# Performance work log

Hardware: AMD Instinct MI355X
Metric: run time of the kernel (lower is better)

Reference implementation:

```python
import jax, jax.numpy as jnp
import numpy as np

N_SRC, N_DST, N_EDGES = 50000, 50000, 500000
IN_DIM, OUT_DIM, EDGE_DIM = 128, 128, 11
BN_EPS = 1e-5


def setup_inputs() -> dict:
    key = jax.random.key(0)
    ks = jax.random.split(key, 16)
    s = 0.05
    return {
        "src_feat": jax.random.normal(ks[0], (N_SRC, IN_DIM), jnp.float32),
        "dst_feat": jax.random.normal(ks[1], (N_DST, IN_DIM), jnp.float32),
        "edge_feats": jax.random.normal(ks[2], (N_EDGES, EDGE_DIM), jnp.float32),
        "src_idx": jax.random.randint(ks[3], (N_EDGES,), 0, N_SRC, jnp.int32),
        "dst_idx": jax.random.randint(ks[4], (N_EDGES,), 0, N_DST, jnp.int32),
        "W_src": jax.random.normal(ks[5], (IN_DIM, OUT_DIM), jnp.float32) * s,
        "b_src": jnp.zeros((OUT_DIM,), jnp.float32),
        "W_dst": jax.random.normal(ks[6], (IN_DIM, OUT_DIM), jnp.float32) * s,
        "b_dst": jnp.zeros((OUT_DIM,), jnp.float32),
        "W_edge": jax.random.normal(ks[7], (EDGE_DIM, OUT_DIM), jnp.float32) * s,
        "b_edge": jnp.zeros((OUT_DIM,), jnp.float32),
        "attn_w": jax.random.normal(ks[8], (3 * OUT_DIM,), jnp.float32) * s,
        "attn_b": jnp.zeros((), jnp.float32),
        "gamma": jnp.ones((OUT_DIM,), jnp.float32),
        "beta": jnp.zeros((OUT_DIM,), jnp.float32),
        "alpha": jnp.asarray(0.25, jnp.float32),
    }


def reference(src_feat, dst_feat, edge_feats, src_idx, dst_idx,
              W_src, b_src, W_dst, b_dst, W_edge, b_edge,
              attn_w, attn_b, gamma, beta, alpha):
    D = W_src.shape[1]
    # project at node/edge level (math identical to projecting gathered feats)
    hs = src_feat @ W_src + b_src            # [Ns, D]  (linear_src)
    hd = dst_feat @ W_dst + b_dst            # [Nd, D]  (linear_dst)
    ep = edge_feats @ W_edge + b_edge        # [E, D]   (linear_edge)
    # attn_l on concat([src, dst, edge]) == sum of three dot products + bias
    aw_s, aw_d, aw_e = attn_w[:D], attn_w[D:2 * D], attn_w[2 * D:]
    a = (hs @ aw_s)[src_idx] + (hd @ aw_d)[dst_idx] + ep @ aw_e + attn_b  # [E]
    # edge softmax over incoming edges of each dst node
    n_dst = dst_feat.shape[0]
    seg_max = jax.ops.segment_max(a, dst_idx, num_segments=n_dst)
    a_exp = jnp.exp(a - seg_max[dst_idx])
    denom = jax.ops.segment_sum(a_exp, dst_idx, num_segments=n_dst)
    attn = a_exp / denom[dst_idx]            # [E]
    # weighted message = attn * linear_src(src_h); scatter-sum to dst
    msg = attn[:, None] * hs[src_idx]        # [E, D]
    h_new = jax.ops.segment_sum(msg, dst_idx, num_segments=n_dst)  # [Nd, D]
    # BatchNorm1d (training-mode batch statistics)
    mean = jnp.mean(h_new, axis=0)
    var = jnp.var(h_new, axis=0)
    h_bn = (h_new - mean) / jnp.sqrt(var + BN_EPS) * gamma + beta
    # PReLU (single shared alpha); dropout is identity in eval
    return jnp.where(h_bn >= 0, h_bn, alpha * h_bn)
```

## Files before the change

### kernel.cpp

```cpp
#include <hip/hip_runtime.h>
#include <cstddef>

#define NSRC 50000
#define NDST 50000
#define NEDGE 500000
#define DIM 128
#define EDIM 11
#define BN_EPS 1e-5f
#define SCAN_NBLK ((NDST + 255) / 256)

#define HS_BLOCKS ((NSRC + 63) / 64)
#define SCB       ((NSRC + 127) / 128)
#define EDB       ((NEDGE + 511) / 512)
#define SC_BLOCKS ((NEDGE + 1023) / 1024)
#define FUSE_GRID (196 * 13)

typedef short bf16x8 __attribute__((ext_vector_type(8)));
typedef float f32x4 __attribute__((ext_vector_type(4)));

#define OFF_HS       0
#define OFF_SSCORE   (OFF_HS + (size_t)NSRC*DIM/2)
#define OFF_DSCORE   (OFF_SSCORE + NSRC)
#define OFF_DEG16    (OFF_DSCORE + NDST)
#define OFF_COLSUM   (OFF_DEG16 + (size_t)NDST*16)
#define OFF_COLSQ    (OFF_COLSUM + 128)
#define OFF_OFFS     (OFF_COLSQ + 128)
#define OFF_EER      (OFF_OFFS + NDST + 2)
#define OFF_PAIRS    (OFF_EER + 2*(size_t)NEDGE)
#define OFF_WDVEC    (OFF_PAIRS + 2*(size_t)NEDGE)
#define OFF_WEVEC    (OFF_WDVEC + 128)
#define OFF_SCAL     (OFF_WEVEC + 16)
#define OFF_WSVEC    (OFF_SCAL + 4)
#define OFF_PART     (OFF_WSVEC + 128)
#define OFF_WT       (((OFF_PART + 256 + 3) / 4) * 4)

__device__ __forceinline__ unsigned short f2bf(float x) {
    unsigned int u = __float_as_uint(x);
    u += 0x7FFFu + ((u >> 16) & 1u);
    return (unsigned short)(u >> 16);
}
__device__ __forceinline__ float bf2f(unsigned int u16) {
    return __uint_as_float(u16 << 16);
}

__global__ __launch_bounds__(256) void k_prepwt(const float* __restrict__ W_dst,
                                                const float* __restrict__ b_dst,
                                                const float* __restrict__ W_edge,
                                                const float* __restrict__ b_edge,
                                                const float* __restrict__ W_src,
                                                const float* __restrict__ b_src,
                                                const float* __restrict__ attn_w,
                                                const float* __restrict__ attn_b,
                                                float* __restrict__ wd_vec,
                                                float* __restrict__ we_vec,
                                                float* __restrict__ ws_vec,
                                                float* __restrict__ scal,
                                                unsigned short* __restrict__ wt) {
    int bb = blockIdx.x;
    int t = threadIdx.x;
    __shared__ float red[128];
    __shared__ float tile[32][33];
    if (bb == 0) {
        if (t < 128) {
            float acc = 0.f;
            for (int d = 0; d < DIM; ++d) acc += W_dst[t * DIM + d] * attn_w[DIM + d];
            wd_vec[t] = acc;
            red[t] = b_dst[t] * attn_w[DIM + t];
        }
        __syncthreads();
        for (int s = 64; s > 0; s >>= 1) { if (t < s) red[t] += red[t + s]; __syncthreads(); }
        if (t == 0) scal[0] = red[0];
    } else if (bb == 1) {
        if (t < 128) {
            if (t < EDIM) {
                float e = 0.f;
                for (int d = 0; d < DIM; ++d) e += W_edge[t * DIM + d] * attn_w[2 * DIM + d];
                we_vec[t] = e;
            }
            red[t] = b_edge[t] * attn_w[2 * DIM + t];
        }
        __syncthreads();
        for (int s = 64; s > 0; s >>= 1) { if (t < s) red[t] += red[t + s]; __syncthreads(); }
        if (t == 0) scal[1] = red[0] + attn_b[0];
    } else if (bb == 2) {
        if (t < 128) {
            float acc = 0.f;
            for (int d = 0; d < DIM; ++d) acc += W_src[t * DIM + d] * attn_w[d];
            ws_vec[t] = acc;
            red[t] = b_src[t] * attn_w[t];
        }
        __syncthreads();
        for (int s = 64; s > 0; s >>= 1) { if (t < s) red[t] += red[t + s]; __syncthreads(); }
        if (t == 0) scal[2] = red[0];
    } else {
        int idx = bb - 3;
        int bi = idx & 3;
        int bj = idx >> 2;
        int cl = t & 31;
        #pragma unroll
        for (int i = 0; i < 4; ++i) {
            int kl = (t >> 5) * 4 + i;
            tile[kl][cl] = W_src[(size_t)(bi * 32 + kl) * DIM + bj * 32 + cl];
        }
        __syncthreads();
        int ko = t & 31;
        #pragma unroll
        for (int i = 0; i < 4; ++i) {
            int co = (t >> 5) * 4 + i;
            wt[(size_t)(bj * 32 + co) * DIM + bi * 32 + ko] = f2bf(tile[ko][co]);
        }
    }
}

__global__ __launch_bounds__(256, 2) void k_fused(const float* __restrict__ A,
                                               const unsigned short* __restrict__ wt,
                                               const float* __restrict__ bias,
                                               const float* __restrict__ ef,
                                               const float* __restrict__ dst_feat,
                                               const int* __restrict__ dst_idx,
                                               const float* __restrict__ ws_vec,
                                               const float* __restrict__ wd_vec,
                                               const float* __restrict__ we_vec,
                                               const float* __restrict__ scal,
                                               unsigned short* __restrict__ hsb,
                                               float* __restrict__ s_score,
                                               float* __restrict__ d_score,
                                               int2* __restrict__ eer,
                                               int* __restrict__ deg16) {
    const int g = blockIdx.x / 13;
    const int sl = blockIdx.x % 13;
    const int t = threadIdx.x;

    if (sl < 4) {
        const int hb = g * 4 + sl;
        if (hb >= HS_BLOCKS) return;
        const int wv = t >> 6;
        const int lane = t & 63;
        const int lrow = lane & 15;
        const int kg = lane >> 4;
        const int grow = hb * 64 + wv * 16 + lrow;
        const bool rowok = grow < NSRC;
        const float* arow = A + (size_t)grow * DIM;

        bf16x8 af[4];
        #pragma unroll
        for (int s = 0; s < 4; ++s) {
            float4 p0 = make_float4(0.f, 0.f, 0.f, 0.f), p1 = p0;
            if (rowok) {
                p0 = *reinterpret_cast<const float4*>(arow + 32 * s + kg * 8);
                p1 = *reinterpret_cast<const float4*>(arow + 32 * s + kg * 8 + 4);
            }
            bf16x8 a;
            a[0] = (short)f2bf(p0.x); a[1] = (short)f2bf(p0.y);
            a[2] = (short)f2bf(p0.z); a[3] = (short)f2bf(p0.w);
            a[4] = (short)f2bf(p1.x); a[5] = (short)f2bf(p1.y);
            a[6] = (short)f2bf(p1.z); a[7] = (short)f2bf(p1.w);
            af[s] = a;
        }

        f32x4 acc[8];
        #pragma unroll
        for (int c = 0; c < 8; ++c) acc[c] = (f32x4){0.f, 0.f, 0.f, 0.f};

        #pragma unroll
        for (int c = 0; c < 8; ++c) {
            #pragma unroll
            for (int s = 0; s < 4; ++s) {
                const bf16x8 b = *reinterpret_cast<const bf16x8*>(
                    wt + ((size_t)(16 * c + lrow) * DIM + 32 * s + kg * 8));
                acc[c] = __builtin_amdgcn_mfma_f32_16x16x32_bf16(af[s], b, acc[c], 0, 0, 0);
            }
        }

        const int orow0 = hb * 64 + wv * 16 + kg * 4;
        #pragma unroll
        for (int c = 0; c < 8; ++c) {
            float bb = bias[16 * c + lrow];
            #pragma unroll
            for (int i = 0; i < 4; ++i) {
                unsigned int mybf = f2bf(acc[c][i] + bb);
                unsigned int nb = (unsigned int)__shfl_xor((int)mybf, 1);
                int orow = orow0 + i;
                if ((lrow & 1) == 0 && orow < NSRC) {
                    *reinterpret_cast<unsigned int*>(hsb + (size_t)orow * DIM + 16 * c + lrow)
                        = (mybf & 0xFFFFu) | (nb << 16);
                }
            }
        }
    } else if (sl < 8) {
        int idx = g * 4 + (sl - 4);
        const float* X;
        const float* V;
        float* out;
        float c;
        if (idx < SCB) {
            X = A; V = ws_vec; out = s_score; c = scal[2];
        } else {
            idx -= SCB;
            if (idx >= SCB) return;
            X = dst_feat; V = wd_vec; out = d_score; c = scal[0];
        }
        int row = idx * 128 + (t >> 1);
        int c0 = (t & 1) * 64;
        if (row >= NDST) return;
        const float4* x = reinterpret_cast<const float4*>(X + (size_t)row * DIM + c0);
        const float4* w = reinterpret_cast<const float4*>(V + c0);
        float p = 0.f;
        #pragma unroll
        for (int i = 0; i < 16; ++i) {
            float4 a = x[i], b = w[i];
            p += a.x * b.x + a.y * b.y + a.z * b.z + a.w * b.w;
        }
        p += __shfl_xor(p, 1);
        if ((t & 1) == 0) out[row] = p + c;
    } else {
        const int eb = g * 5 + (sl - 8);
        if (eb >= EDB) return;
        float wvv[EDIM];
        #pragma unroll
        for (int k = 0; k < EDIM; ++k) wvv[k] = we_vec[k];
        const float s1 = scal[1];
        int ebase = eb * 512 + t;
        #pragma unroll
        for (int i = 0; i < 2; ++i) {
            int e = ebase + i * 256;
            if (e < NEDGE) {
                int d = dst_idx[e];
                const float* er = ef + (size_t)e * EDIM;
                float a = s1;
                #pragma unroll
                for (int k = 0; k < EDIM; ++k) a += er[k] * wvv[k];
                int r = atomicAdd(&deg16[(size_t)d * 16], 1);
                eer[e] = make_int2(r, __float_as_int(a));
            }
        }
    }
}

__global__ __launch_bounds__(256) void k_scanA(const int* __restrict__ deg16,
                                               int* __restrict__ offL,
                                               int* __restrict__ partials) {
    __shared__ int tmp[256];
    int t = threadIdx.x;
    int i = blockIdx.x * 256 + t;
    int v = (i < NDST) ? deg16[(size_t)i * 16] : 0;
    tmp[t] = v;
    __syncthreads();
    #pragma unroll
    for (int d = 1; d < 256; d <<= 1) {
        int u = (t >= d) ? tmp[t - d] : 0;
        __syncthreads();
        tmp[t] += u;
        __syncthreads();
    }
    if (i < NDST) offL[i] = tmp[t] - v;
    if (t == 255) partials[blockIdx.x] = tmp[255];
}

__global__ __launch_bounds__(256) void k_scanB(int* __restrict__ partials) {
    __shared__ int tmp[256];
    int t = threadIdx.x;
    int v = (t < SCAN_NBLK) ? partials[t] : 0;
    tmp[t] = v;
    __syncthreads();
    #pragma unroll
    for (int d = 1; d < 256; d <<= 1) {
        int u = (t >= d) ? tmp[t - d] : 0;
        __syncthreads();
        tmp[t] += u;
        __syncthreads();
    }
    if (t < SCAN_NBLK) partials[t] = tmp[t] - v;
}

__global__ __launch_bounds__(256) void k_scat(const int* __restrict__ src_idx,
                                              const int* __restrict__ dst_idx,
                                              const int2* __restrict__ eer,
                                              const float* __restrict__ s_score,
                                              const float* __restrict__ d_score,
                                              const int* __restrict__ offL,
                                              const int* __restrict__ part,
                                              int2* __restrict__ pairs) {
    int base = blockIdx.x * 1024 + threadIdx.x;
    #pragma unroll
    for (int i = 0; i < 4; ++i) {
        int e = base + i * 256;
        if (e < NEDGE) {
            int s = src_idx[e], d = dst_idx[e];
            int2 re = eer[e];
            float w = expf(__int_as_float(re.y) + s_score[s] + d_score[d]);
            int pos = offL[d] + part[d >> 8] + re.x;
            pairs[pos] = make_int2(s, __float_as_int(w));
        }
    }
}

__global__ __launch_bounds__(256) void k_gather(const unsigned short* __restrict__ hsb,
                                                const int* __restrict__ offL,
                                                const int* __restrict__ part,
                                                const int2* __restrict__ pairs,
                                                float* __restrict__ h_new) {
    int wid = (blockIdx.x * blockDim.x + threadIdx.x) >> 6;
    int lane = threadIdx.x & 63;
    if (wid >= NDST) return;
    int b = offL[wid] + part[wid >> 8];
    int e2 = (wid + 1 < NDST) ? (offL[wid + 1] + part[(wid + 1) >> 8]) : NEDGE;
    int deg = e2 - b;
    const int half = lane >> 5;
    const int c8 = lane & 31;
    float a0 = 0.f, a1 = 0.f, a2 = 0.f, a3 = 0.f, wsum = 0.f;

    for (int base = 0; base < deg; base += 64) {
        int cnt = min(deg - base, 64);
        int myS = 0;
        float myW = 0.f;
        if (lane < cnt) {
            int2 p = pairs[b + base + lane];
            myS = p.x;
            myW = __int_as_float(p.y);
        }
        wsum += myW;

        int j = 0;
        for (; j + 8 <= cnt; j += 8) {
            #pragma unroll
            for (int q = 0; q < 4; ++q) {
                int jj = j + 2 * q + half;
                int s0 = __shfl(myS, jj);
                float w0 = __shfl(myW, jj);
                uint2 v = *reinterpret_cast<const uint2*>(hsb + (size_t)s0 * DIM + c8 * 4);
                a0 += w0 * bf2f(v.x & 0xFFFFu);
                a1 += w0 * bf2f(v.x >> 16);
                a2 += w0 * bf2f(v.y & 0xFFFFu);
                a3 += w0 * bf2f(v.y >> 16);
            }
        }
        for (; j < cnt; j += 2) {
            int jj = j + half;
            int s0 = __shfl(myS, jj);
            float w0 = __shfl(myW, jj);
            uint2 v = *reinterpret_cast<const uint2*>(hsb + (size_t)s0 * DIM + c8 * 4);
            a0 += w0 * bf2f(v.x & 0xFFFFu);
            a1 += w0 * bf2f(v.x >> 16);
            a2 += w0 * bf2f(v.y & 0xFFFFu);
            a3 += w0 * bf2f(v.y >> 16);
        }
    }

    a0 += __shfl_xor(a0, 32);
    a1 += __shfl_xor(a1, 32);
    a2 += __shfl_xor(a2, 32);
    a3 += __shfl_xor(a3, 32);
    #pragma unroll
    for (int m = 1; m < 64; m <<= 1) wsum += __shfl_xor(wsum, m);

    float inv = (deg > 0) ? 1.f / wsum : 0.f;
    if (half == 0) {
        reinterpret_cast<float4*>(h_new + (size_t)wid * DIM)[c8]
            = make_float4(a0 * inv, a1 * inv, a2 * inv, a3 * inv);
    }
}

__global__ __launch_bounds__(256) void k_bnstats(const float* __restrict__ h,
                                                 float* __restrict__ colsum,
                                                 float* __restrict__ colsq) {
    int col = threadIdx.x & 127;
    int rp = threadIdx.x >> 7;
    float s = 0.f, q = 0.f;
    for (int r = blockIdx.x * 2 + rp; r < NDST; r += gridDim.x * 2) {
        float x = h[(size_t)r * DIM + col];
        s += x;
        q += x * x;
    }
    __shared__ float ls[2][128], lq[2][128];
    ls[rp][col] = s;
    lq[rp][col] = q;
    __syncthreads();
    if (rp == 0) {
        atomicAdd(&colsum[col], ls[0][col] + ls[1][col]);
        atomicAdd(&colsq[col], lq[0][col] + lq[1][col]);
    }
}

__global__ __launch_bounds__(256) void k_bnfinal(float* __restrict__ h,
                                                 const float* __restrict__ colsum,
                                                 const float* __restrict__ colsq,
                                                 const float* __restrict__ gamma,
                                                 const float* __restrict__ beta,
                                                 const float* __restrict__ alpha_p) {
    const size_t total4 = (size_t)NDST * DIM / 4;
    const float alpha = alpha_p[0];
    const float invN = 1.f / (float)NDST;
    const int c0 = (threadIdx.x & 31) * 4;
    float sc[4], sh[4];
    #pragma unroll
    for (int k = 0; k < 4; ++k) {
        float mean = colsum[c0 + k] * invN;
        float var = colsq[c0 + k] * invN - mean * mean;
        float s = gamma[c0 + k] * rsqrtf(var + BN_EPS);
        sc[k] = s;
        sh[k] = beta[c0 + k] - mean * s;
    }
    size_t stride = (size_t)gridDim.x * blockDim.x;
    for (size_t i = blockIdx.x * blockDim.x + threadIdx.x; i < total4; i += stride) {
        float4 x = reinterpret_cast<float4*>(h)[i];
        float y0 = x.x * sc[0] + sh[0];
        float y1 = x.y * sc[1] + sh[1];
        float y2 = x.z * sc[2] + sh[2];
        float y3 = x.w * sc[3] + sh[3];
        float4 o;
        o.x = y0 >= 0.f ? y0 : alpha * y0;
        o.y = y1 >= 0.f ? y1 : alpha * y1;
        o.z = y2 >= 0.f ? y2 : alpha * y2;
        o.w = y3 >= 0.f ? y3 : alpha * y3;
        reinterpret_cast<float4*>(h)[i] = o;
    }
}

extern "C" void kernel_launch(void* const* d_in, const int* in_sizes, int n_in,
                              void* d_out, int out_size, void* d_ws, size_t ws_size,
                              hipStream_t stream) {
    const float* src_feat   = (const float*)d_in[0];
    const float* dst_feat   = (const float*)d_in[1];
    const float* edge_feats = (const float*)d_in[2];
    const int*   src_idx    = (const int*)d_in[3];
    const int*   dst_idx    = (const int*)d_in[4];
    const float* W_src      = (const float*)d_in[5];
    const float* b_src      = (const float*)d_in[6];
    const float* W_dst      = (const float*)d_in[7];
    const float* b_dst      = (const float*)d_in[8];
    const float* W_edge     = (const float*)d_in[9];
    const float* b_edge     = (const float*)d_in[10];
    const float* attn_w     = (const float*)d_in[11];
    const float* attn_b     = (const float*)d_in[12];
    const float* gamma      = (const float*)d_in[13];
    const float* beta       = (const float*)d_in[14];
    const float* alpha      = (const float*)d_in[15];

    float* ws      = (float*)d_ws;
    unsigned short* hsb = (unsigned short*)(ws + OFF_HS);
    float* s_score = ws + OFF_SSCORE;
    float* d_score = ws + OFF_DSCORE;
    int*   deg16   = (int*)(ws + OFF_DEG16);
    float* colsum  = ws + OFF_COLSUM;
    float* colsq   = ws + OFF_COLSQ;
    int*   offL    = (int*)(ws + OFF_OFFS);
    int2*  eer     = (int2*)(ws + OFF_EER);
    int2*  pairs   = (int2*)(ws + OFF_PAIRS);
    float* wd_vec  = ws + OFF_WDVEC;
    float* we_vec  = ws + OFF_WEVEC;
    float* scal    = ws + OFF_SCAL;
    float* ws_vec  = ws + OFF_WSVEC;
    int*   part    = (int*)(ws + OFF_PART);
    unsigned short* wt = (unsigned short*)(ws + OFF_WT);

    float* h_new = (float*)d_out;

    hipMemsetAsync(deg16, 0, ((size_t)NDST * 16 + 256) * sizeof(int), stream);

    k_prepwt<<<19, 256, 0, stream>>>(W_dst, b_dst, W_edge, b_edge, W_src, b_src,
                                     attn_w, attn_b, wd_vec, we_vec, ws_vec, scal, wt);
    k_fused<<<FUSE_GRID, 256, 0, stream>>>(src_feat, wt, b_src, edge_feats,
                                           dst_feat, dst_idx, ws_vec, wd_vec,
                                           we_vec, scal, hsb, s_score, d_score,
                                           eer, deg16);
    k_scanA<<<SCAN_NBLK, 256, 0, stream>>>(deg16, offL, part);
    k_scanB<<<1, 256, 0, stream>>>(part);
    k_scat<<<SC_BLOCKS, 256, 0, stream>>>(src_idx, dst_idx, eer, s_score, d_score,
                                          offL, part, pairs);
    k_gather<<<(NDST * 64 + 255) / 256, 256, 0, stream>>>(hsb, offL, part, pairs, h_new);
    k_bnstats<<<512, 256, 0, stream>>>(h_new, colsum, colsq);
    k_bnfinal<<<1024, 256, 0, stream>>>(h_new, colsum, colsq, gamma, beta, alpha);
}
```

Baseline: 134.9 us.

## Fuse scan, scatter, gather and batchnorm into one persistent kernel with grid barriers

```diff
diff --git a/kernel.cpp b/kernel.cpp
--- a/kernel.cpp
+++ b/kernel.cpp
@@ -12,8 +12,8 @@
 #define HS_BLOCKS ((NSRC + 63) / 64)
 #define SCB       ((NSRC + 127) / 128)
 #define EDB       ((NEDGE + 511) / 512)
-#define SC_BLOCKS ((NEDGE + 1023) / 1024)
 #define FUSE_GRID (196 * 13)
+#define TAILB 768
 
 typedef short bf16x8 __attribute__((ext_vector_type(8)));
 typedef float f32x4 __attribute__((ext_vector_type(4)));
@@ -24,7 +24,8 @@
 #define OFF_DEG16    (OFF_DSCORE + NDST)
 #define OFF_COLSUM   (OFF_DEG16 + (size_t)NDST*16)
 #define OFF_COLSQ    (OFF_COLSUM + 128)
-#define OFF_OFFS     (OFF_COLSQ + 128)
+#define OFF_BAR      (OFF_COLSQ + 128)
+#define OFF_OFFS     (OFF_BAR + 64)
 #define OFF_EER      (OFF_OFFS + NDST + 2)
 #define OFF_PAIRS    (OFF_EER + 2*(size_t)NEDGE)
 #define OFF_WDVEC    (OFF_PAIRS + 2*(size_t)NEDGE)
@@ -41,6 +42,18 @@
 }
 __device__ __forceinline__ float bf2f(unsigned int u16) {
     return __uint_as_float(u16 << 16);
+}
+
+__device__ __forceinline__ void gbar(int* bar, int idx) {
+    __syncthreads();
+    if (threadIdx.x == 0) {
+        __threadfence();
+        atomicAdd(&bar[idx * 16], 1);
+        while (atomicAdd(&bar[idx * 16], 0) < TAILB)
+            __builtin_amdgcn_s_sleep(8);
+        __threadfence();
+    }
+    __syncthreads();
 }
 
 __global__ __launch_bounds__(256) void k_prepwt(const float* __restrict__ W_dst,
@@ -237,183 +250,180 @@
     }
 }
 
-__global__ __launch_bounds__(256) void k_scanA(const int* __restrict__ deg16,
-                                               int* __restrict__ offL,
-                                               int* __restrict__ partials) {
-    __shared__ int tmp[256];
-    int t = threadIdx.x;
-    int i = blockIdx.x * 256 + t;
-    int v = (i < NDST) ? deg16[(size_t)i * 16] : 0;
-    tmp[t] = v;
-    __syncthreads();
-    #pragma unroll
-    for (int d = 1; d < 256; d <<= 1) {
-        int u = (t >= d) ? tmp[t - d] : 0;
-        __syncthreads();
-        tmp[t] += u;
-        __syncthreads();
-    }
-    if (i < NDST) offL[i] = tmp[t] - v;
-    if (t == 255) partials[blockIdx.x] = tmp[255];
-}
-
-__global__ __launch_bounds__(256) void k_scanB(int* __restrict__ partials) {
-    __shared__ int tmp[256];
-    int t = threadIdx.x;
-    int v = (t < SCAN_NBLK) ? partials[t] : 0;
-    tmp[t] = v;
-    __syncthreads();
-    #pragma unroll
-    for (int d = 1; d < 256; d <<= 1) {
-        int u = (t >= d) ? tmp[t - d] : 0;
-        __syncthreads();
-        tmp[t] += u;
-        __syncthreads();
-    }
-    if (t < SCAN_NBLK) partials[t] = tmp[t] - v;
-}
-
-__global__ __launch_bounds__(256) void k_scat(const int* __restrict__ src_idx,
-                                              const int* __restrict__ dst_idx,
-                                              const int2* __restrict__ eer,
-                                              const float* __restrict__ s_score,
-                                              const float* __restrict__ d_score,
-                                              const int* __restrict__ offL,
-                                              const int* __restrict__ part,
-                                              int2* __restrict__ pairs) {
-    int base = blockIdx.x * 1024 + threadIdx.x;
-    #pragma unroll
-    for (int i = 0; i < 4; ++i) {
-        int e = base + i * 256;
-        if (e < NEDGE) {
-            int s = src_idx[e], d = dst_idx[e];
-            int2 re = eer[e];
-            float w = expf(__int_as_float(re.y) + s_score[s] + d_score[d]);
-            int pos = offL[d] + part[d >> 8] + re.x;
-            pairs[pos] = make_int2(s, __float_as_int(w));
-        }
-    }
-}
-
-__global__ __launch_bounds__(256) void k_gather(const unsigned short* __restrict__ hsb,
-                                                const int* __restrict__ offL,
-                                                const int* __restrict__ part,
-                                                const int2* __restrict__ pairs,
-                                                float* __restrict__ h_new) {
-    int wid = (blockIdx.x * blockDim.x + threadIdx.x) >> 6;
-    int lane = threadIdx.x & 63;
-    if (wid >= NDST) return;
-    int b = offL[wid] + part[wid >> 8];
-    int e2 = (wid + 1 < NDST) ? (offL[wid + 1] + part[(wid + 1) >> 8]) : NEDGE;
-    int deg = e2 - b;
-    const int half = lane >> 5;
-    const int c8 = lane & 31;
-    float a0 = 0.f, a1 = 0.f, a2 = 0.f, a3 = 0.f, wsum = 0.f;
-
-    for (int base = 0; base < deg; base += 64) {
-        int cnt = min(deg - base, 64);
-        int myS = 0;
-        float myW = 0.f;
-        if (lane < cnt) {
-            int2 p = pairs[b + base + lane];
-            myS = p.x;
-            myW = __int_as_float(p.y);
-        }
-        wsum += myW;
-
-        int j = 0;
-        for (; j + 8 <= cnt; j += 8) {
-            #pragma unroll
-            for (int q = 0; q < 4; ++q) {
-                int jj = j + 2 * q + half;
-                int s0 = __shfl(myS, jj);
-                float w0 = __shfl(myW, jj);
-                uint2 v = *reinterpret_cast<const uint2*>(hsb + (size_t)s0 * DIM + c8 * 4);
-                a0 += w0 * bf2f(v.x & 0xFFFFu);
-                a1 += w0 * bf2f(v.x >> 16);
-                a2 += w0 * bf2f(v.y & 0xFFFFu);
-                a3 += w0 * bf2f(v.y >> 16);
-            }
-        }
-        for (; j < cnt; j += 2) {
-            int jj = j + half;
-            int s0 = __shfl(myS, jj);
-            float w0 = __shfl(myW, jj);
-            uint2 v = *reinterpret_cast<const uint2*>(hsb + (size_t)s0 * DIM + c8 * 4);
-            a0 += w0 * bf2f(v.x & 0xFFFFu);
-            a1 += w0 * bf2f(v.x >> 16);
-            a2 += w0 * bf2f(v.y & 0xFFFFu);
-            a3 += w0 * bf2f(v.y >> 16);
-        }
-    }
-
-    a0 += __shfl_xor(a0, 32);
-    a1 += __shfl_xor(a1, 32);
-    a2 += __shfl_xor(a2, 32);
-    a3 += __shfl_xor(a3, 32);
-    #pragma unroll
-    for (int m = 1; m < 64; m <<= 1) wsum += __shfl_xor(wsum, m);
-
-    float inv = (deg > 0) ? 1.f / wsum : 0.f;
-    if (half == 0) {
-        reinterpret_cast<float4*>(h_new + (size_t)wid * DIM)[c8]
-            = make_float4(a0 * inv, a1 * inv, a2 * inv, a3 * inv);
-    }
-}
-
-__global__ __launch_bounds__(256) void k_bnstats(const float* __restrict__ h,
+__global__ __launch_bounds__(256, 4) void k_tail(const int* __restrict__ src_idx,
+                                                 const int* __restrict__ dst_idx,
+                                                 const int2* __restrict__ eer,
+                                                 const float* __restrict__ s_score,
+                                                 const float* __restrict__ d_score,
+                                                 const int* __restrict__ deg16,
+                                                 int* __restrict__ offL,
+                                                 int* __restrict__ partraw,
+                                                 int2* __restrict__ pairs,
+                                                 const unsigned short* __restrict__ hsb,
+                                                 float* __restrict__ h_new,
                                                  float* __restrict__ colsum,
-                                                 float* __restrict__ colsq) {
-    int col = threadIdx.x & 127;
-    int rp = threadIdx.x >> 7;
-    float s = 0.f, q = 0.f;
-    for (int r = blockIdx.x * 2 + rp; r < NDST; r += gridDim.x * 2) {
-        float x = h[(size_t)r * DIM + col];
-        s += x;
-        q += x * x;
-    }
-    __shared__ float ls[2][128], lq[2][128];
-    ls[rp][col] = s;
-    lq[rp][col] = q;
-    __syncthreads();
-    if (rp == 0) {
-        atomicAdd(&colsum[col], ls[0][col] + ls[1][col]);
-        atomicAdd(&colsq[col], lq[0][col] + lq[1][col]);
-    }
-}
-
-__global__ __launch_bounds__(256) void k_bnfinal(float* __restrict__ h,
-                                                 const float* __restrict__ colsum,
-                                                 const float* __restrict__ colsq,
+                                                 float* __restrict__ colsq,
                                                  const float* __restrict__ gamma,
                                                  const float* __restrict__ beta,
-                                                 const float* __restrict__ alpha_p) {
-    const size_t total4 = (size_t)NDST * DIM / 4;
-    const float alpha = alpha_p[0];
-    const float invN = 1.f / (float)NDST;
-    const int c0 = (threadIdx.x & 31) * 4;
-    float sc[4], sh[4];
-    #pragma unroll
-    for (int k = 0; k < 4; ++k) {
-        float mean = colsum[c0 + k] * invN;
-        float var = colsq[c0 + k] * invN - mean * mean;
-        float s = gamma[c0 + k] * rsqrtf(var + BN_EPS);
-        sc[k] = s;
-        sh[k] = beta[c0 + k] - mean * s;
-    }
-    size_t stride = (size_t)gridDim.x * blockDim.x;
-    for (size_t i = blockIdx.x * blockDim.x + threadIdx.x; i < total4; i += stride) {
-        float4 x = reinterpret_cast<float4*>(h)[i];
-        float y0 = x.x * sc[0] + sh[0];
-        float y1 = x.y * sc[1] + sh[1];
-        float y2 = x.z * sc[2] + sh[2];
-        float y3 = x.w * sc[3] + sh[3];
-        float4 o;
-        o.x = y0 >= 0.f ? y0 : alpha * y0;
-        o.y = y1 >= 0.f ? y1 : alpha * y1;
-        o.z = y2 >= 0.f ? y2 : alpha * y2;
-        o.w = y3 >= 0.f ? y3 : alpha * y3;
-        reinterpret_cast<float4*>(h)[i] = o;
+                                                 const float* __restrict__ alpha_p,
+                                                 int* bar) {
+    const int t = threadIdx.x;
+    const int bid = blockIdx.x;
+    __shared__ int tmp[256];
+    __shared__ int partS[256];
+    __shared__ float ls[2][128], lq[2][128];
+
+    if (bid < SCAN_NBLK) {
+        int i = bid * 256 + t;
+        int v = (i < NDST) ? deg16[(size_t)i * 16] : 0;
+        tmp[t] = v;
+        __syncthreads();
+        #pragma unroll
+        for (int d = 1; d < 256; d <<= 1) {
+            int u = (t >= d) ? tmp[t - d] : 0;
+            __syncthreads();
+            tmp[t] += u;
+            __syncthreads();
+        }
+        if (i < NDST) offL[i] = tmp[t] - v;
+        if (t == 255) partraw[bid] = tmp[255];
+    }
+    gbar(bar, 0);
+
+    {
+        int v = (t < SCAN_NBLK) ? partraw[t] : 0;
+        tmp[t] = v;
+        __syncthreads();
+        #pragma unroll
+        for (int d = 1; d < 256; d <<= 1) {
+            int u = (t >= d) ? tmp[t - d] : 0;
+            __syncthreads();
+            tmp[t] += u;
+            __syncthreads();
+        }
+        partS[t] = tmp[t] - v;
+        __syncthreads();
+    }
+
+    for (int e = bid * 256 + t; e < NEDGE; e += TAILB * 256) {
+        int s = src_idx[e], d = dst_idx[e];
+        int2 re = eer[e];
+        float w = expf(__int_as_float(re.y) + s_score[s] + d_score[d]);
+        int pos = offL[d] + partS[d >> 8] + re.x;
+        pairs[pos] = make_int2(s, __float_as_int(w));
+    }
+    gbar(bar, 1);
+
+    {
+        const int lane = t & 63;
+        const int half = lane >> 5;
+        const int c8 = lane & 31;
+        for (int wid = bid * 4 + (t >> 6); wid < NDST; wid += TAILB * 4) {
+            int b = offL[wid] + partS[wid >> 8];
+            int e2 = (wid + 1 < NDST) ? (offL[wid + 1] + partS[(wid + 1) >> 8]) : NEDGE;
+            int deg = e2 - b;
+            float a0 = 0.f, a1 = 0.f, a2 = 0.f, a3 = 0.f, wsum = 0.f;
+
+            for (int base = 0; base < deg; base += 64) {
+                int cnt = min(deg - base, 64);
+                int myS = 0;
+                float myW = 0.f;
+                if (lane < cnt) {
+                    int2 p = pairs[b + base + lane];
+                    myS = p.x;
+                    myW = __int_as_float(p.y);
+                }
+                wsum += myW;
+
+                int j = 0;
+                for (; j + 8 <= cnt; j += 8) {
+                    #pragma unroll
+                    for (int q = 0; q < 4; ++q) {
+                        int jj = j + 2 * q + half;
+                        int s0 = __shfl(myS, jj);
+                        float w0 = __shfl(myW, jj);
+                        uint2 v = *reinterpret_cast<const uint2*>(hsb + (size_t)s0 * DIM + c8 * 4);
+                        a0 += w0 * bf2f(v.x & 0xFFFFu);
+                        a1 += w0 * bf2f(v.x >> 16);
+                        a2 += w0 * bf2f(v.y & 0xFFFFu);
+                        a3 += w0 * bf2f(v.y >> 16);
+                    }
+                }
+                for (; j < cnt; j += 2) {
+                    int jj = j + half;
+                    int s0 = __shfl(myS, jj);
+                    float w0 = __shfl(myW, jj);
+                    uint2 v = *reinterpret_cast<const uint2*>(hsb + (size_t)s0 * DIM + c8 * 4);
+                    a0 += w0 * bf2f(v.x & 0xFFFFu);
+                    a1 += w0 * bf2f(v.x >> 16);
+                    a2 += w0 * bf2f(v.y & 0xFFFFu);
+                    a3 += w0 * bf2f(v.y >> 16);
+                }
+            }
+
+            a0 += __shfl_xor(a0, 32);
+            a1 += __shfl_xor(a1, 32);
+            a2 += __shfl_xor(a2, 32);
+            a3 += __shfl_xor(a3, 32);
+            #pragma unroll
+            for (int m = 1; m < 64; m <<= 1) wsum += __shfl_xor(wsum, m);
+
+            float inv = (deg > 0) ? 1.f / wsum : 0.f;
+            if (half == 0) {
+                reinterpret_cast<float4*>(h_new + (size_t)wid * DIM)[c8]
+                    = make_float4(a0 * inv, a1 * inv, a2 * inv, a3 * inv);
+            }
+        }
+    }
+    gbar(bar, 2);
+
+    {
+        int col = t & 127;
+        int rp = t >> 7;
+        float s = 0.f, q = 0.f;
+        for (int r = bid * 2 + rp; r < NDST; r += TAILB * 2) {
+            float x = h_new[(size_t)r * DIM + col];
+            s += x;
+            q += x * x;
+        }
+        ls[rp][col] = s;
+        lq[rp][col] = q;
+        __syncthreads();
+        if (rp == 0) {
+            atomicAdd(&colsum[col], ls[0][col] + ls[1][col]);
+            atomicAdd(&colsq[col], lq[0][col] + lq[1][col]);
+        }
+    }
+    gbar(bar, 3);
+
+    {
+        const size_t total4 = (size_t)NDST * DIM / 4;
+        const float alpha = alpha_p[0];
+        const float invN = 1.f / (float)NDST;
+        const int c0 = (t & 31) * 4;
+        float sc[4], sh[4];
+        #pragma unroll
+        for (int k = 0; k < 4; ++k) {
+            float mean = colsum[c0 + k] * invN;
+            float var = colsq[c0 + k] * invN - mean * mean;
+            float s = gamma[c0 + k] * rsqrtf(var + BN_EPS);
+            sc[k] = s;
+            sh[k] = beta[c0 + k] - mean * s;
+        }
+        size_t stride = (size_t)TAILB * 256;
+        for (size_t i = (size_t)bid * 256 + t; i < total4; i += stride) {
+            float4 x = reinterpret_cast<float4*>(h_new)[i];
+            float y0 = x.x * sc[0] + sh[0];
+            float y1 = x.y * sc[1] + sh[1];
+            float y2 = x.z * sc[2] + sh[2];
+            float y3 = x.w * sc[3] + sh[3];
+            float4 o;
+            o.x = y0 >= 0.f ? y0 : alpha * y0;
+            o.y = y1 >= 0.f ? y1 : alpha * y1;
+            o.z = y2 >= 0.f ? y2 : alpha * y2;
+            o.w = y3 >= 0.f ? y3 : alpha * y3;
+            reinterpret_cast<float4*>(h_new)[i] = o;
+        }
     }
 }
 
@@ -444,6 +454,7 @@
     int*   deg16   = (int*)(ws + OFF_DEG16);
     float* colsum  = ws + OFF_COLSUM;
     float* colsq   = ws + OFF_COLSQ;
+    int*   bar     = (int*)(ws + OFF_BAR);
     int*   offL    = (int*)(ws + OFF_OFFS);
     int2*  eer     = (int2*)(ws + OFF_EER);
     int2*  pairs   = (int2*)(ws + OFF_PAIRS);
@@ -451,12 +462,12 @@
     float* we_vec  = ws + OFF_WEVEC;
     float* scal    = ws + OFF_SCAL;
     float* ws_vec  = ws + OFF_WSVEC;
-    int*   part    = (int*)(ws + OFF_PART);
+    int*   partraw = (int*)(ws + OFF_PART);
     unsigned short* wt = (unsigned short*)(ws + OFF_WT);
 
     float* h_new = (float*)d_out;
 
-    hipMemsetAsync(deg16, 0, ((size_t)NDST * 16 + 256) * sizeof(int), stream);
+    hipMemsetAsync(deg16, 0, ((size_t)NDST * 16 + 128 + 128 + 64) * sizeof(int), stream);
 
     k_prepwt<<<19, 256, 0, stream>>>(W_dst, b_dst, W_edge, b_edge, W_src, b_src,
                                      attn_w, attn_b, wd_vec, we_vec, ws_vec, scal, wt);
@@ -464,11 +475,7 @@
                                            dst_feat, dst_idx, ws_vec, wd_vec,
                                            we_vec, scal, hsb, s_score, d_score,
                                            eer, deg16);
-    k_scanA<<<SCAN_NBLK, 256, 0, stream>>>(deg16, offL, part);
-    k_scanB<<<1, 256, 0, stream>>>(part);
-    k_scat<<<SC_BLOCKS, 256, 0, stream>>>(src_idx, dst_idx, eer, s_score, d_score,
-                                          offL, part, pairs);
-    k_gather<<<(NDST * 64 + 255) / 256, 256, 0, stream>>>(hsb, offL, part, pairs, h_new);
-    k_bnstats<<<512, 256, 0, stream>>>(h_new, colsum, colsq);
-    k_bnfinal<<<1024, 256, 0, stream>>>(h_new, colsum, colsq, gamma, beta, alpha);
-}
+    k_tail<<<TAILB, 256, 0, stream>>>(src_idx, dst_idx, eer, s_score, d_score,
+                                      deg16, offL, partraw, pairs, hsb, h_new,
+                                      colsum, colsq, gamma, beta, alpha, bar);
+}
```

Measured after the change: 461.3 us. +241.8%, slower.
